# Optimization experiments

Hardware: AMD Instinct MI355X
Metric: run time of the kernel (lower is better)

## Reference

```python
import jax, jax.numpy as jnp
import numpy as np

N = 50000   # num_nodes
E = 800000  # num edges (COO)
T = 50      # timesteps
H = 64      # hidden_units


def setup_inputs() -> dict:
    key = jax.random.key(0)
    ks = jax.random.split(key, 16)
    s = 0.1  # weight init scale
    return {
        "features": jax.random.normal(ks[0], (1, T, N), jnp.float32),
        "index": jax.random.randint(ks[1], (E, 2), 0, N, jnp.int32),
        "value": jax.random.uniform(ks[2], (E,), jnp.float32),
        "W1_g": jax.random.normal(ks[3], (1 + H, 2 * H), jnp.float32) * s,
        "b1_g": jnp.ones((2 * H,), jnp.float32),
        "W1_c": jax.random.normal(ks[4], (1 + H, H), jnp.float32) * s,
        "b1_c": jnp.zeros((H,), jnp.float32),
        "W2b_g": jax.random.normal(ks[5], (H + 1, 2), jnp.float32) * s,
        "b2b_g": jnp.ones((2,), jnp.float32),
        "W2b_c": jax.random.normal(ks[6], (H + 1, 1), jnp.float32) * s,
        "b2b_c": jnp.zeros((1,), jnp.float32),
        "W2u_g": jax.random.normal(ks[7], (H + 1, 2), jnp.float32) * s,
        "b2u_g": jnp.ones((2,), jnp.float32),
        "W2u_c": jax.random.normal(ks[8], (H + 1, 1), jnp.float32) * s,
        "b2u_c": jnp.zeros((1,), jnp.float32),
    }


def _spmm(rows, cols, vals, X):
    # sparse COO adjacency (rows, cols, vals) @ dense X [N, d]
    return jax.ops.segment_sum(vals[:, None] * X[cols], rows, num_segments=N)


def _gru_layer(xs, rows, cols, vals, Wg, bg, Wc, bc, units):
    # xs: [T, N, d_in]; GCN-GRU cell scanned over time, batch=1
    h0 = jnp.zeros((N, units), xs.dtype)

    def step(h, x):
        def gconv(st, W, b):
            xc = jnp.concatenate([x, st], axis=-1)     # [N, d_in+units]
            return _spmm(rows, cols, vals, xc) @ W + b  # [N, out]

        ru = jax.nn.sigmoid(gconv(h, Wg, bg))
        r, u = jnp.split(ru, 2, axis=-1)
        c = jnp.tanh(gconv(r * h, Wc, bc))
        hn = u * h + (1.0 - u) * c
        return hn, hn

    _, hs = jax.lax.scan(step, h0, xs)
    return hs  # [T, N, units]


def reference(features, index, value, W1_g, b1_g, W1_c, b1_c,
              W2b_g, b2b_g, W2b_c, b2b_c, W2u_g, b2u_g, W2u_c, b2u_c):
    rows, cols = index[:, 0], index[:, 1]
    xs = features[0][..., None]  # [T, N, 1]
    # shared first layer (cell_1 is used by both multi-cell stacks)
    h1 = _gru_layer(xs, rows, cols, value, W1_g, b1_g, W1_c, b1_c, H)  # [T,N,H]
    out_b = _gru_layer(h1, rows, cols, value, W2b_g, b2b_g, W2b_c, b2b_c, 1)
    out_u = _gru_layer(h1, rows, cols, value, W2u_g, b2u_g, W2u_c, b2u_c, 1)
    # dynamic_rnn outputs: [batch=1, T, N]
    return out_b[..., 0][None], out_u[..., 0][None]
```

## Files before the change

### kernel.cpp

```cpp
#include <hip/hip_runtime.h>
#include <math.h>

#define NN 50000
#define EE 800000
#define TT 50

__device__ __forceinline__ float sigm(float x)   { return 1.f / (1.f + __expf(-x)); }
__device__ __forceinline__ float tanh_f(float x) { float e = __expf(2.f * x); return 1.f - 2.f / (e + 1.f); }


__global__ __launch_bounds__(256) void hist_kernel(const int* __restrict__ idx, int* __restrict__ cnt) {
    int e = blockIdx.x * blockDim.x + threadIdx.x;
    if (e < EE) atomicAdd(&cnt[idx[2 * e]], 1);
}

__global__ __launch_bounds__(1024) void scan_kernel(const int* __restrict__ cnt, int* __restrict__ rp) {
    __shared__ int part[1024];
    const int PER = (NN + 1023) / 1024;
    int t = threadIdx.x;
    int base = t * PER;
    int s = 0;
    for (int i = 0; i < PER; ++i) {
        int idx = base + i;
        if (idx < NN) s += cnt[idx];
    }
    part[t] = s;
    __syncthreads();
    int v = s;
    for (int off = 1; off < 1024; off <<= 1) {
        int add = (t >= off) ? part[t - off] : 0;
        __syncthreads();
        v += add;
        part[t] = v;
        __syncthreads();
    }
    int run = v - s;
    if (t == 0) rp[0] = 0;
    for (int i = 0; i < PER; ++i) {
        int idx = base + i;
        if (idx < NN) { run += cnt[idx]; rp[idx + 1] = run; }
    }
}

__global__ __launch_bounds__(256) void scatter_kernel(const int* __restrict__ idx, const float* __restrict__ val,
                                                      const int* __restrict__ rp, int* __restrict__ cnt,
                                                      int2* __restrict__ ev) {
    int e = blockIdx.x * blockDim.x + threadIdx.x;
    if (e >= EE) return;
    int r = idx[2 * e];
    int p = rp[r] + atomicAdd(&cnt[r], 1);
    ev[p] = make_int2(idx[2 * e + 1], __float_as_int(val[e]));
}


__global__ __launch_bounds__(256) void transpose_x(const float* __restrict__ F, float* __restrict__ xT) {
    __shared__ float tile[64][51];
    int n0 = blockIdx.x * 64;
    for (int i = threadIdx.x; i < TT * 64; i += 256) {
        int t = i >> 6, n = i & 63;
        if (n0 + n < NN) tile[n][t] = F[(size_t)t * NN + n0 + n];
    }
    __syncthreads();
    for (int i = threadIdx.x; i < 64 * 64; i += 256) {
        int n = i >> 6, t = i & 63;
        if (n0 + n < NN) xT[(size_t)(n0 + n) * 64 + t] = (t < TT) ? tile[n][t] : 0.f;
    }
}

__global__ __launch_bounds__(256) void spmm_sx(const int* __restrict__ rp, const int2* __restrict__ ev,
                                               const float* __restrict__ xT, float* __restrict__ SxAll) {
    int w = __builtin_amdgcn_readfirstlane((blockIdx.x * blockDim.x + threadIdx.x) >> 6);
    int lane = threadIdx.x & 63;
    if (w >= NN) return;
    int e0 = __builtin_amdgcn_readfirstlane(rp[w]);
    int e1 = __builtin_amdgcn_readfirstlane(rp[w + 1]);
    const float* xl = xT + lane;
    float a0 = 0.f, a1 = 0.f, a2 = 0.f, a3 = 0.f, a4 = 0.f, a5 = 0.f, a6 = 0.f, a7 = 0.f;
    int e = e0;
    for (; e + 8 <= e1; e += 8) {
        int2 q0 = ev[e + 0], q1 = ev[e + 1], q2 = ev[e + 2], q3 = ev[e + 3];
        int2 q4 = ev[e + 4], q5 = ev[e + 5], q6 = ev[e + 6], q7 = ev[e + 7];
        a0 = fmaf(__int_as_float(q0.y), xl[(size_t)q0.x * 64], a0);
        a1 = fmaf(__int_as_float(q1.y), xl[(size_t)q1.x * 64], a1);
        a2 = fmaf(__int_as_float(q2.y), xl[(size_t)q2.x * 64], a2);
        a3 = fmaf(__int_as_float(q3.y), xl[(size_t)q3.x * 64], a3);
        a4 = fmaf(__int_as_float(q4.y), xl[(size_t)q4.x * 64], a4);
        a5 = fmaf(__int_as_float(q5.y), xl[(size_t)q5.x * 64], a5);
        a6 = fmaf(__int_as_float(q6.y), xl[(size_t)q6.x * 64], a6);
        a7 = fmaf(__int_as_float(q7.y), xl[(size_t)q7.x * 64], a7);
    }
    for (; e < e1; ++e) {
        int2 q = ev[e];
        a0 = fmaf(__int_as_float(q.y), xl[(size_t)q.x * 64], a0);
    }
    float s = ((a0 + a1) + (a2 + a3)) + ((a4 + a5) + (a6 + a7));
    if (lane < TT) SxAll[(size_t)lane * NN + w] = s;
}


__global__ __launch_bounds__(256) void spmm64(const int* __restrict__ rp, const int2* __restrict__ ev,
                                              const float* __restrict__ Xin, float* __restrict__ Sout) {
    int w = __builtin_amdgcn_readfirstlane((blockIdx.x * blockDim.x + threadIdx.x) >> 6);
    int lane = threadIdx.x & 63;
    if (w >= NN) return;
    int e0 = __builtin_amdgcn_readfirstlane(rp[w]);
    int e1 = __builtin_amdgcn_readfirstlane(rp[w + 1]);
    const float* xl = Xin + lane;
    float a0 = 0.f, a1 = 0.f, a2 = 0.f, a3 = 0.f, a4 = 0.f, a5 = 0.f, a6 = 0.f, a7 = 0.f;
    int e = e0;
    for (; e + 8 <= e1; e += 8) {
        int2 q0 = ev[e + 0], q1 = ev[e + 1], q2 = ev[e + 2], q3 = ev[e + 3];
        int2 q4 = ev[e + 4], q5 = ev[e + 5], q6 = ev[e + 6], q7 = ev[e + 7];
        a0 = fmaf(__int_as_float(q0.y), xl[(size_t)q0.x * 64], a0);
        a1 = fmaf(__int_as_float(q1.y), xl[(size_t)q1.x * 64], a1);
        a2 = fmaf(__int_as_float(q2.y), xl[(size_t)q2.x * 64], a2);
        a3 = fmaf(__int_as_float(q3.y), xl[(size_t)q3.x * 64], a3);
        a4 = fmaf(__int_as_float(q4.y), xl[(size_t)q4.x * 64], a4);
        a5 = fmaf(__int_as_float(q5.y), xl[(size_t)q5.x * 64], a5);
        a6 = fmaf(__int_as_float(q6.y), xl[(size_t)q6.x * 64], a6);
        a7 = fmaf(__int_as_float(q7.y), xl[(size_t)q7.x * 64], a7);
    }
    for (; e < e1; ++e) {
        int2 q = ev[e];
        a0 = fmaf(__int_as_float(q.y), xl[(size_t)q.x * 64], a0);
    }
    Sout[(size_t)w * 64 + lane] = ((a0 + a1) + (a2 + a3)) + ((a4 + a5) + (a6 + a7));
}


__global__ __launch_bounds__(256) void cand_update(const float* __restrict__ S2, const float* __restrict__ Sx,
                                                   const float* __restrict__ Wc, const float* __restrict__ bc,
                                                   const float* __restrict__ u1, float* __restrict__ h1,
                                                   const float* __restrict__ Wbg, const float* __restrict__ Wbc,
                                                   const float* __restrict__ Wug, const float* __restrict__ Wuc,
                                                   float* __restrict__ z8) {
    int j = threadIdx.x & 63;
    int g = threadIdx.x >> 6;
    float w[65];
#pragma unroll
    for (int k = 0; k < 65; ++k) w[k] = Wc[k * 64 + j];
    float bj = bc[j];
    float wz0 = Wbg[j * 2], wz1 = Wbg[j * 2 + 1], wz2 = Wbc[j];
    float wz3 = Wug[j * 2], wz4 = Wug[j * 2 + 1], wz5 = Wuc[j];
    for (int n = blockIdx.x * 4 + g; n < NN; n += gridDim.x * 4) {
        float acc = fmaf(Sx[n], w[0], bj);
        const float4* s2 = (const float4*)(S2 + (size_t)n * 64);
#pragma unroll
        for (int q = 0; q < 16; ++q) {
            float4 sv = s2[q];
            acc = fmaf(sv.x, w[1 + 4 * q], acc);
            acc = fmaf(sv.y, w[2 + 4 * q], acc);
            acc = fmaf(sv.z, w[3 + 4 * q], acc);
            acc = fmaf(sv.w, w[4 + 4 * q], acc);
        }
        float c = tanh_f(acc);
        float u = u1[(size_t)n * 64 + j];
        float ho = h1[(size_t)n * 64 + j];
        float hn = fmaf(u, ho - c, c);
        h1[(size_t)n * 64 + j] = hn;
        float p0 = hn * wz0, p1 = hn * wz1, p2 = hn * wz2;
        float p3 = hn * wz3, p4 = hn * wz4, p5 = hn * wz5;
#pragma unroll
        for (int off = 1; off < 64; off <<= 1) {
            p0 += __shfl_xor(p0, off);
            p1 += __shfl_xor(p1, off);
            p2 += __shfl_xor(p2, off);
            p3 += __shfl_xor(p3, off);
            p4 += __shfl_xor(p4, off);
            p5 += __shfl_xor(p5, off);
        }
        if (j == 0) {
            z8[(size_t)n * 8 + 0] = p0; z8[(size_t)n * 8 + 1] = p1; z8[(size_t)n * 8 + 2] = p2;
            z8[(size_t)n * 8 + 3] = p3; z8[(size_t)n * 8 + 4] = p4; z8[(size_t)n * 8 + 5] = p5;
        }
    }
}


__global__ __launch_bounds__(256) void merged1(int GA,
        const int* __restrict__ rp, const int2* __restrict__ ev,
        const float* __restrict__ h1, float* __restrict__ Sh,
        const float* __restrict__ z8,
        const float* __restrict__ hb, const float* __restrict__ hu,
        const float* __restrict__ Wbg, const float* __restrict__ bbg,
        const float* __restrict__ Wug, const float* __restrict__ bug,
        float* __restrict__ z2, float* __restrict__ g2, float* __restrict__ S3c) {
    if ((int)blockIdx.x < GA) {
        int w = __builtin_amdgcn_readfirstlane(((int)blockIdx.x * 256 + (int)threadIdx.x) >> 6);
        int lane = threadIdx.x & 63;
        if (w >= NN) return;
        int e0 = __builtin_amdgcn_readfirstlane(rp[w]);
        int e1 = __builtin_amdgcn_readfirstlane(rp[w + 1]);
        const float* xl = h1 + lane;
        float a0 = 0.f, a1 = 0.f, a2 = 0.f, a3 = 0.f, a4 = 0.f, a5 = 0.f, a6 = 0.f, a7 = 0.f;
        int e = e0;
        for (; e + 8 <= e1; e += 8) {
            int2 q0 = ev[e + 0], q1 = ev[e + 1], q2 = ev[e + 2], q3 = ev[e + 3];
            int2 q4 = ev[e + 4], q5 = ev[e + 5], q6 = ev[e + 6], q7 = ev[e + 7];
            a0 = fmaf(__int_as_float(q0.y), xl[(size_t)q0.x * 64], a0);
            a1 = fmaf(__int_as_float(q1.y), xl[(size_t)q1.x * 64], a1);
            a2 = fmaf(__int_as_float(q2.y), xl[(size_t)q2.x * 64], a2);
            a3 = fmaf(__int_as_float(q3.y), xl[(size_t)q3.x * 64], a3);
            a4 = fmaf(__int_as_float(q4.y), xl[(size_t)q4.x * 64], a4);
            a5 = fmaf(__int_as_float(q5.y), xl[(size_t)q5.x * 64], a5);
            a6 = fmaf(__int_as_float(q6.y), xl[(size_t)q6.x * 64], a6);
            a7 = fmaf(__int_as_float(q7.y), xl[(size_t)q7.x * 64], a7);
        }
        for (; e < e1; ++e) {
            int2 q = ev[e];
            a0 = fmaf(__int_as_float(q.y), xl[(size_t)q.x * 64], a0);
        }
        Sh[(size_t)w * 64 + lane] = ((a0 + a1) + (a2 + a3)) + ((a4 + a5) + (a6 + a7));
    } else {
        int gid = ((int)blockIdx.x - GA) * 256 + threadIdx.x;
        int row = gid >> 3;
        int j = gid & 7;
        if (row >= NN) return;
        int e = rp[row], e1 = rp[row + 1];
        float a0 = 0.f, a1 = 0.f, a2 = 0.f, a3 = 0.f;
        for (; e + 3 < e1; e += 4) {
            int2 p0 = ev[e], p1 = ev[e + 1], p2 = ev[e + 2], p3 = ev[e + 3];
            a0 = fmaf(__int_as_float(p0.y), z8[(size_t)p0.x * 8 + j], a0);
            a1 = fmaf(__int_as_float(p1.y), z8[(size_t)p1.x * 8 + j], a1);
            a2 = fmaf(__int_as_float(p2.y), z8[(size_t)p2.x * 8 + j], a2);
            a3 = fmaf(__int_as_float(p3.y), z8[(size_t)p3.x * 8 + j], a3);
        }
        for (; e < e1; ++e) {
            int2 p = ev[e];
            a0 = fmaf(__int_as_float(p.y), z8[(size_t)p.x * 8 + j], a0);
        }
        float s = (a0 + a1) + (a2 + a3);
        if (j == 2) S3c[row * 2 + 0] = s;
        if (j == 5) S3c[row * 2 + 1] = s;
        int lane = threadIdx.x & 63;
        int base = lane & ~7;
        float s0 = __shfl(s, base + 0);
        float s1 = __shfl(s, base + 1);
        float s3 = __shfl(s, base + 3);
        float s4 = __shfl(s, base + 4);
        float s6 = __shfl(s, base + 6);
        float s7 = __shfl(s, base + 7);
        if (j == 0) {
            float rb = sigm(fmaf(s6, Wbg[128], s0) + bbg[0]);
            float ub = sigm(fmaf(s6, Wbg[129], s1) + bbg[1]);
            float ru = sigm(fmaf(s7, Wug[128], s3) + bug[0]);
            float uu = sigm(fmaf(s7, Wug[129], s4) + bug[1]);
            z2[row * 2 + 0] = rb * hb[row];
            z2[row * 2 + 1] = ru * hu[row];
            g2[row * 2 + 0] = ub;
            g2[row * 2 + 1] = uu;
        }
    }
}


#define G1_CHUNK 32
__global__ __launch_bounds__(128) void merged2(int GA,
        const float* __restrict__ Sh, const float* __restrict__ Sx,
        const float* __restrict__ Wg, const float* __restrict__ bg,
        const float* __restrict__ h1, float* __restrict__ rh, float* __restrict__ u1,
        const int* __restrict__ rp, const int2* __restrict__ ev,
        const float* __restrict__ z2, const float* __restrict__ S3c, const float* __restrict__ g2,
        const float* __restrict__ Wbc, const float* __restrict__ bbc,
        const float* __restrict__ Wuc, const float* __restrict__ buc,
        float* __restrict__ hb, float* __restrict__ hu,
        float* __restrict__ z8, float* __restrict__ out, int tPrev) {
    __shared__ float4 s4[G1_CHUNK][16];
    __shared__ float sxl[G1_CHUNK];
    if ((int)blockIdx.x < GA) {
        int j = threadIdx.x;
        float w0 = Wg[j];
        float wk[64];
#pragma unroll
        for (int k = 0; k < 64; ++k) wk[k] = Wg[(1 + k) * 128 + j];
        float bj = bg[j];
        int n0 = (int)blockIdx.x * G1_CHUNK;
        int nmax = min(G1_CHUNK, NN - n0);
        for (int idx = j; idx < G1_CHUNK * 16; idx += 128) {
            int n = idx >> 4, q = idx & 15;
            if (n < nmax) s4[n][q] = *(const float4*)(Sh + (size_t)(n0 + n) * 64 + q * 4);
        }
        if (j < G1_CHUNK && j < nmax) sxl[j] = Sx[n0 + j];
        __syncthreads();
        for (int n = 0; n < nmax; ++n) {
            float acc = fmaf(sxl[n], w0, bj);
#pragma unroll
            for (int q = 0; q < 16; ++q) {
                float4 sv = s4[n][q];
                acc = fmaf(sv.x, wk[4 * q + 0], acc);
                acc = fmaf(sv.y, wk[4 * q + 1], acc);
                acc = fmaf(sv.z, wk[4 * q + 2], acc);
                acc = fmaf(sv.w, wk[4 * q + 3], acc);
            }
            float g = sigm(acc);
            int node = n0 + n;
            if (j < 64) rh[(size_t)node * 64 + j] = g * h1[(size_t)node * 64 + j];
            else        u1[(size_t)node * 64 + (j - 64)] = g;
        }
    } else {
        int gid = ((int)blockIdx.x - GA) * 128 + threadIdx.x;
        int row = gid >> 1;
        int j = gid & 1;
        if (row >= NN) return;
        int e = rp[row], e1 = rp[row + 1];
        float a0 = 0.f, a1 = 0.f, a2 = 0.f, a3 = 0.f;
        for (; e + 3 < e1; e += 4) {
            int2 p0 = ev[e], p1 = ev[e + 1], p2 = ev[e + 2], p3 = ev[e + 3];
            a0 = fmaf(__int_as_float(p0.y), z2[(size_t)p0.x * 2 + j], a0);
            a1 = fmaf(__int_as_float(p1.y), z2[(size_t)p1.x * 2 + j], a1);
            a2 = fmaf(__int_as_float(p2.y), z2[(size_t)p2.x * 2 + j], a2);
            a3 = fmaf(__int_as_float(p3.y), z2[(size_t)p3.x * 2 + j], a3);
        }
        for (; e < e1; ++e) {
            int2 p = ev[e];
            a0 = fmaf(__int_as_float(p.y), z2[(size_t)p.x * 2 + j], a0);
        }
        float s = (a0 + a1) + (a2 + a3);
        int lane = threadIdx.x & 63;
        int base = lane & ~1;
        float sA = __shfl(s, base + 0);
        float sB = __shfl(s, base + 1);
        if (j == 0) {
            float cb = tanh_f(fmaf(sA, Wbc[64], S3c[row * 2 + 0]) + bbc[0]);
            float cu = tanh_f(fmaf(sB, Wuc[64], S3c[row * 2 + 1]) + buc[0]);
            float ub = g2[row * 2 + 0], uu = g2[row * 2 + 1];
            float hbn = fmaf(ub, hb[row] - cb, cb);
            float hun = fmaf(uu, hu[row] - cu, cu);
            hb[row] = hbn; hu[row] = hun;
            z8[(size_t)row * 8 + 6] = hbn;
            z8[(size_t)row * 8 + 7] = hun;
            out[(size_t)tPrev * NN + row] = hbn;
            out[(size_t)(TT + tPrev) * NN + row] = hun;
        }
    }
}


extern "C" void kernel_launch(void* const* d_in, const int* in_sizes, int n_in,
                              void* d_out, int out_size, void* d_ws, size_t ws_size,
                              hipStream_t stream) {
    const float* features = (const float*)d_in[0];
    const int*   index    = (const int*)d_in[1];
    const float* value    = (const float*)d_in[2];
    const float* W1g  = (const float*)d_in[3];
    const float* b1g  = (const float*)d_in[4];
    const float* W1c  = (const float*)d_in[5];
    const float* b1c  = (const float*)d_in[6];
    const float* W2bg = (const float*)d_in[7];
    const float* b2bg = (const float*)d_in[8];
    const float* W2bc = (const float*)d_in[9];
    const float* b2bc = (const float*)d_in[10];
    const float* W2ug = (const float*)d_in[11];
    const float* b2ug = (const float*)d_in[12];
    const float* W2uc = (const float*)d_in[13];
    const float* b2uc = (const float*)d_in[14];
    float* out = (float*)d_out;

    char* ws = (char*)d_ws;
    size_t o = 0;
    auto alloc = [&](size_t bytes) { size_t cur = o; o += (bytes + 255) & ~(size_t)255; return cur; };
    size_t o_h1  = alloc((size_t)NN * 64 * 4);
    size_t o_hb  = alloc((size_t)NN * 4);
    size_t o_hu  = alloc((size_t)NN * 4);
    size_t o_z8  = alloc((size_t)NN * 8 * 4);
    size_t zeroEnd = o;
    size_t o_rp  = alloc((size_t)(NN + 1) * 4);
    size_t o_cnt = alloc((size_t)NN * 4);
    size_t o_ev  = alloc((size_t)EE * 8);
    size_t o_Sh  = alloc((size_t)NN * 64 * 4);
    size_t o_SxA = alloc((size_t)TT * NN * 4);
    size_t o_rh  = alloc((size_t)NN * 64 * 4);
    size_t o_u1  = alloc((size_t)NN * 64 * 4);
    size_t o_S2  = alloc((size_t)NN * 64 * 4);
    size_t o_S3c = alloc((size_t)NN * 2 * 4);
    size_t o_z2  = alloc((size_t)NN * 2 * 4);
    size_t o_g2  = alloc((size_t)NN * 2 * 4);
    (void)ws_size; (void)in_sizes; (void)n_in; (void)out_size;

    float* h1  = (float*)(ws + o_h1);
    float* hb  = (float*)(ws + o_hb);
    float* hu  = (float*)(ws + o_hu);
    float* z8  = (float*)(ws + o_z8);
    int*   rp  = (int*)(ws + o_rp);
    int*   cnt = (int*)(ws + o_cnt);
    int2*  ev  = (int2*)(ws + o_ev);
    float* Sh  = (float*)(ws + o_Sh);
    float* SxA = (float*)(ws + o_SxA);
    float* rh  = (float*)(ws + o_rh);
    float* u1  = (float*)(ws + o_u1);
    float* S2  = (float*)(ws + o_S2);
    float* S3c = (float*)(ws + o_S3c);
    float* z2  = (float*)(ws + o_z2);
    float* g2  = (float*)(ws + o_g2);
    float* xT  = S2;

    (void)hipMemsetAsync(ws + o_cnt, 0, (size_t)NN * 4, stream);
    hist_kernel<<<(EE + 255) / 256, 256, 0, stream>>>(index, cnt);
    scan_kernel<<<1, 1024, 0, stream>>>(cnt, rp);
    (void)hipMemsetAsync(ws + o_cnt, 0, (size_t)NN * 4, stream);
    scatter_kernel<<<(EE + 255) / 256, 256, 0, stream>>>(index, value, rp, cnt, ev);

    (void)hipMemsetAsync(ws + o_h1, 0, zeroEnd - o_h1, stream);
    (void)hipMemsetAsync(ws + o_Sh, 0, (size_t)NN * 64 * 4, stream);

    transpose_x<<<(NN + 63) / 64, 256, 0, stream>>>(features, xT);
    spmm_sx<<<(NN + 3) / 4, 256, 0, stream>>>(rp, ev, xT, SxA);

    const int GA1 = (NN + 3) / 4;
    const int GB1 = (NN * 8 + 255) / 256;
    const int GA2 = (NN + G1_CHUNK - 1) / G1_CHUNK;
    const int GB2 = (NN * 2 + 127) / 128;

    for (int t = 0; t < TT; ++t) {
        const float* Sxt = SxA + (size_t)t * NN;
        int g2grid = (t > 0) ? (GA2 + GB2) : GA2;
        merged2<<<g2grid, 128, 0, stream>>>(GA2, Sh, Sxt, W1g, b1g, h1, rh, u1,
                                            rp, ev, z2, S3c, g2, W2bc, b2bc, W2uc, b2uc,
                                            hb, hu, z8, out, t - 1);
        spmm64<<<(NN + 3) / 4, 256, 0, stream>>>(rp, ev, rh, S2);
        cand_update<<<1024, 256, 0, stream>>>(S2, Sxt, W1c, b1c, u1, h1, W2bg, W2bc, W2ug, W2uc, z8);
        int gA = (t < TT - 1) ? GA1 : 0;
        merged1<<<gA + GB1, 256, 0, stream>>>(gA, rp, ev, h1, Sh,
                                              z8, hb, hu, W2bg, b2bg, W2ug, b2ug, z2, g2, S3c);
    }
    merged2<<<GB2, 128, 0, stream>>>(0, Sh, SxA, W1g, b1g, h1, rh, u1,
                                     rp, ev, z2, S3c, g2, W2bc, b2bc, W2uc, b2uc,
                                     hb, hu, z8, out, TT - 1);
}
```

Baseline: 7.534 ms.

## Fuse candidate SpMM with GRU update and pad CSR rows to multiples of eight

Each CSR row is padded to a multiple of 8 entries. The padding slots are zero-filled, so they read column 0 with weight 0. This lets every SpMM drop its scalar tail loop. The separate spmm64 and cand_update kernels are merged into one spmm_cand kernel: each wave computes its row's aggregated r*h in LDS and immediately applies the candidate weights, which are also held in LDS. That removes the S2 buffer round trip and one launch per timestep. The single-block prefix scan is also replaced with a three-kernel block scan, at the cost of roughly a fifth more gather traffic from the padding entries.

```diff
diff --git a/kernel.cpp b/kernel.cpp
--- a/kernel.cpp
+++ b/kernel.cpp
@@ -4,6 +4,8 @@
 #define NN 50000
 #define EE 800000
 #define TT 50
+#define EVCAP 1150016
+#define SB 196
 
 __device__ __forceinline__ float sigm(float x)   { return 1.f / (1.f + __expf(-x)); }
 __device__ __forceinline__ float tanh_f(float x) { float e = __expf(2.f * x); return 1.f - 2.f / (e + 1.f); }
@@ -14,32 +16,46 @@
     if (e < EE) atomicAdd(&cnt[idx[2 * e]], 1);
 }
 
-__global__ __launch_bounds__(1024) void scan_kernel(const int* __restrict__ cnt, int* __restrict__ rp) {
-    __shared__ int part[1024];
-    const int PER = (NN + 1023) / 1024;
+__global__ __launch_bounds__(256) void scan1(const int* __restrict__ cnt, int* __restrict__ rp,
+                                             int* __restrict__ bsum) {
+    __shared__ int s[256];
     int t = threadIdx.x;
-    int base = t * PER;
-    int s = 0;
-    for (int i = 0; i < PER; ++i) {
-        int idx = base + i;
-        if (idx < NN) s += cnt[idx];
-    }
-    part[t] = s;
+    int g = blockIdx.x * 256 + t;
+    int v = (g < NN) ? ((cnt[g] + 7) & ~7) : 0;
+    s[t] = v;
     __syncthreads();
-    int v = s;
-    for (int off = 1; off < 1024; off <<= 1) {
-        int add = (t >= off) ? part[t - off] : 0;
+    for (int off = 1; off < 256; off <<= 1) {
+        int add = (t >= off) ? s[t - off] : 0;
         __syncthreads();
         v += add;
-        part[t] = v;
+        s[t] = v;
         __syncthreads();
     }
-    int run = v - s;
-    if (t == 0) rp[0] = 0;
-    for (int i = 0; i < PER; ++i) {
-        int idx = base + i;
-        if (idx < NN) { run += cnt[idx]; rp[idx + 1] = run; }
-    }
+    if (g < NN) rp[g + 1] = v;
+    if (t == 255) bsum[blockIdx.x] = v;
+}
+
+__global__ __launch_bounds__(256) void scan2(int* __restrict__ bsum) {
+    __shared__ int s[256];
+    int t = threadIdx.x;
+    int v = (t < SB) ? bsum[t] : 0;
+    s[t] = v;
+    __syncthreads();
+    for (int off = 1; off < 256; off <<= 1) {
+        int add = (t >= off) ? s[t - off] : 0;
+        __syncthreads();
+        v += add;
+        s[t] = v;
+        __syncthreads();
+    }
+    if (t < SB) bsum[t] = v;
+}
+
+__global__ __launch_bounds__(256) void scan3(int* __restrict__ rp, const int* __restrict__ bsum) {
+    int g = blockIdx.x * 256 + threadIdx.x;
+    int off = (blockIdx.x > 0) ? bsum[blockIdx.x - 1] : 0;
+    if (g < NN) rp[g + 1] += off;
+    if (g == 0) rp[0] = 0;
 }
 
 __global__ __launch_bounds__(256) void scatter_kernel(const int* __restrict__ idx, const float* __restrict__ val,
@@ -72,12 +88,11 @@
     int w = __builtin_amdgcn_readfirstlane((blockIdx.x * blockDim.x + threadIdx.x) >> 6);
     int lane = threadIdx.x & 63;
     if (w >= NN) return;
-    int e0 = __builtin_amdgcn_readfirstlane(rp[w]);
+    int e  = __builtin_amdgcn_readfirstlane(rp[w]);
     int e1 = __builtin_amdgcn_readfirstlane(rp[w + 1]);
     const float* xl = xT + lane;
     float a0 = 0.f, a1 = 0.f, a2 = 0.f, a3 = 0.f, a4 = 0.f, a5 = 0.f, a6 = 0.f, a7 = 0.f;
-    int e = e0;
-    for (; e + 8 <= e1; e += 8) {
+    for (; e < e1; e += 8) {
         int2 q0 = ev[e + 0], q1 = ev[e + 1], q2 = ev[e + 2], q3 = ev[e + 3];
         int2 q4 = ev[e + 4], q5 = ev[e + 5], q6 = ev[e + 6], q7 = ev[e + 7];
         a0 = fmaf(__int_as_float(q0.y), xl[(size_t)q0.x * 64], a0);
@@ -89,75 +104,60 @@
         a6 = fmaf(__int_as_float(q6.y), xl[(size_t)q6.x * 64], a6);
         a7 = fmaf(__int_as_float(q7.y), xl[(size_t)q7.x * 64], a7);
     }
-    for (; e < e1; ++e) {
-        int2 q = ev[e];
-        a0 = fmaf(__int_as_float(q.y), xl[(size_t)q.x * 64], a0);
-    }
     float s = ((a0 + a1) + (a2 + a3)) + ((a4 + a5) + (a6 + a7));
     if (lane < TT) SxAll[(size_t)lane * NN + w] = s;
 }
 
 
-__global__ __launch_bounds__(256) void spmm64(const int* __restrict__ rp, const int2* __restrict__ ev,
-                                              const float* __restrict__ Xin, float* __restrict__ Sout) {
-    int w = __builtin_amdgcn_readfirstlane((blockIdx.x * blockDim.x + threadIdx.x) >> 6);
-    int lane = threadIdx.x & 63;
-    if (w >= NN) return;
-    int e0 = __builtin_amdgcn_readfirstlane(rp[w]);
-    int e1 = __builtin_amdgcn_readfirstlane(rp[w + 1]);
-    const float* xl = Xin + lane;
-    float a0 = 0.f, a1 = 0.f, a2 = 0.f, a3 = 0.f, a4 = 0.f, a5 = 0.f, a6 = 0.f, a7 = 0.f;
-    int e = e0;
-    for (; e + 8 <= e1; e += 8) {
-        int2 q0 = ev[e + 0], q1 = ev[e + 1], q2 = ev[e + 2], q3 = ev[e + 3];
-        int2 q4 = ev[e + 4], q5 = ev[e + 5], q6 = ev[e + 6], q7 = ev[e + 7];
-        a0 = fmaf(__int_as_float(q0.y), xl[(size_t)q0.x * 64], a0);
-        a1 = fmaf(__int_as_float(q1.y), xl[(size_t)q1.x * 64], a1);
-        a2 = fmaf(__int_as_float(q2.y), xl[(size_t)q2.x * 64], a2);
-        a3 = fmaf(__int_as_float(q3.y), xl[(size_t)q3.x * 64], a3);
-        a4 = fmaf(__int_as_float(q4.y), xl[(size_t)q4.x * 64], a4);
-        a5 = fmaf(__int_as_float(q5.y), xl[(size_t)q5.x * 64], a5);
-        a6 = fmaf(__int_as_float(q6.y), xl[(size_t)q6.x * 64], a6);
-        a7 = fmaf(__int_as_float(q7.y), xl[(size_t)q7.x * 64], a7);
-    }
-    for (; e < e1; ++e) {
-        int2 q = ev[e];
-        a0 = fmaf(__int_as_float(q.y), xl[(size_t)q.x * 64], a0);
-    }
-    Sout[(size_t)w * 64 + lane] = ((a0 + a1) + (a2 + a3)) + ((a4 + a5) + (a6 + a7));
-}
-
-
-__global__ __launch_bounds__(256) void cand_update(const float* __restrict__ S2, const float* __restrict__ Sx,
-                                                   const float* __restrict__ Wc, const float* __restrict__ bc,
-                                                   const float* __restrict__ u1, float* __restrict__ h1,
-                                                   const float* __restrict__ Wbg, const float* __restrict__ Wbc,
-                                                   const float* __restrict__ Wug, const float* __restrict__ Wuc,
-                                                   float* __restrict__ z8) {
-    int j = threadIdx.x & 63;
-    int g = threadIdx.x >> 6;
-    float w[65];
-#pragma unroll
-    for (int k = 0; k < 65; ++k) w[k] = Wc[k * 64 + j];
+__global__ __launch_bounds__(256) void spmm_cand(const int* __restrict__ rp, const int2* __restrict__ ev,
+        const float* __restrict__ rh, const float* __restrict__ Sx,
+        const float* __restrict__ Wc, const float* __restrict__ bc,
+        const float* __restrict__ u1, float* __restrict__ h1,
+        const float* __restrict__ Wbg, const float* __restrict__ Wbc,
+        const float* __restrict__ Wug, const float* __restrict__ Wuc,
+        float* __restrict__ z8) {
+    __shared__ float ldsW[65 * 64];
+    __shared__ float ldsS[4][64];
+    int t = threadIdx.x;
+    for (int i = t; i < 65 * 16; i += 256)
+        ((float4*)ldsW)[i] = ((const float4*)Wc)[i];
+    __syncthreads();
+    int lane = t & 63;
+    int wv = t >> 6;
+    int j = lane;
     float bj = bc[j];
     float wz0 = Wbg[j * 2], wz1 = Wbg[j * 2 + 1], wz2 = Wbc[j];
     float wz3 = Wug[j * 2], wz4 = Wug[j * 2 + 1], wz5 = Wuc[j];
-    for (int n = blockIdx.x * 4 + g; n < NN; n += gridDim.x * 4) {
-        float acc = fmaf(Sx[n], w[0], bj);
-        const float4* s2 = (const float4*)(S2 + (size_t)n * 64);
-#pragma unroll
-        for (int q = 0; q < 16; ++q) {
-            float4 sv = s2[q];
-            acc = fmaf(sv.x, w[1 + 4 * q], acc);
-            acc = fmaf(sv.y, w[2 + 4 * q], acc);
-            acc = fmaf(sv.z, w[3 + 4 * q], acc);
-            acc = fmaf(sv.w, w[4 + 4 * q], acc);
-        }
+    int wstride = gridDim.x * 4;
+    for (int wi = blockIdx.x * 4 + wv; wi < NN; wi += wstride) {
+        int w = __builtin_amdgcn_readfirstlane(wi);
+        int e  = __builtin_amdgcn_readfirstlane(rp[w]);
+        int e1 = __builtin_amdgcn_readfirstlane(rp[w + 1]);
+        const float* xl = rh + lane;
+        float a0 = 0.f, a1 = 0.f, a2 = 0.f, a3 = 0.f, a4 = 0.f, a5 = 0.f, a6 = 0.f, a7 = 0.f;
+        for (; e < e1; e += 8) {
+            int2 q0 = ev[e + 0], q1 = ev[e + 1], q2 = ev[e + 2], q3 = ev[e + 3];
+            int2 q4 = ev[e + 4], q5 = ev[e + 5], q6 = ev[e + 6], q7 = ev[e + 7];
+            a0 = fmaf(__int_as_float(q0.y), xl[(size_t)q0.x * 64], a0);
+            a1 = fmaf(__int_as_float(q1.y), xl[(size_t)q1.x * 64], a1);
+            a2 = fmaf(__int_as_float(q2.y), xl[(size_t)q2.x * 64], a2);
+            a3 = fmaf(__int_as_float(q3.y), xl[(size_t)q3.x * 64], a3);
+            a4 = fmaf(__int_as_float(q4.y), xl[(size_t)q4.x * 64], a4);
+            a5 = fmaf(__int_as_float(q5.y), xl[(size_t)q5.x * 64], a5);
+            a6 = fmaf(__int_as_float(q6.y), xl[(size_t)q6.x * 64], a6);
+            a7 = fmaf(__int_as_float(q7.y), xl[(size_t)q7.x * 64], a7);
+        }
+        float s2 = ((a0 + a1) + (a2 + a3)) + ((a4 + a5) + (a6 + a7));
+        ldsS[wv][lane] = s2;
+        float acc = fmaf(Sx[w], ldsW[j], bj);
+#pragma unroll 8
+        for (int k = 0; k < 64; ++k)
+            acc = fmaf(ldsS[wv][k], ldsW[(k + 1) * 64 + j], acc);
         float c = tanh_f(acc);
-        float u = u1[(size_t)n * 64 + j];
-        float ho = h1[(size_t)n * 64 + j];
+        float u  = u1[(size_t)w * 64 + j];
+        float ho = h1[(size_t)w * 64 + j];
         float hn = fmaf(u, ho - c, c);
-        h1[(size_t)n * 64 + j] = hn;
+        h1[(size_t)w * 64 + j] = hn;
         float p0 = hn * wz0, p1 = hn * wz1, p2 = hn * wz2;
         float p3 = hn * wz3, p4 = hn * wz4, p5 = hn * wz5;
 #pragma unroll
@@ -170,8 +170,8 @@
             p5 += __shfl_xor(p5, off);
         }
         if (j == 0) {
-            z8[(size_t)n * 8 + 0] = p0; z8[(size_t)n * 8 + 1] = p1; z8[(size_t)n * 8 + 2] = p2;
-            z8[(size_t)n * 8 + 3] = p3; z8[(size_t)n * 8 + 4] = p4; z8[(size_t)n * 8 + 5] = p5;
+            z8[(size_t)w * 8 + 0] = p0; z8[(size_t)w * 8 + 1] = p1; z8[(size_t)w * 8 + 2] = p2;
+            z8[(size_t)w * 8 + 3] = p3; z8[(size_t)w * 8 + 4] = p4; z8[(size_t)w * 8 + 5] = p5;
         }
     }
 }
@@ -189,12 +189,11 @@
         int w = __builtin_amdgcn_readfirstlane(((int)blockIdx.x * 256 + (int)threadIdx.x) >> 6);
         int lane = threadIdx.x & 63;
         if (w >= NN) return;
-        int e0 = __builtin_amdgcn_readfirstlane(rp[w]);
+        int e  = __builtin_amdgcn_readfirstlane(rp[w]);
         int e1 = __builtin_amdgcn_readfirstlane(rp[w + 1]);
         const float* xl = h1 + lane;
         float a0 = 0.f, a1 = 0.f, a2 = 0.f, a3 = 0.f, a4 = 0.f, a5 = 0.f, a6 = 0.f, a7 = 0.f;
-        int e = e0;
-        for (; e + 8 <= e1; e += 8) {
+        for (; e < e1; e += 8) {
             int2 q0 = ev[e + 0], q1 = ev[e + 1], q2 = ev[e + 2], q3 = ev[e + 3];
             int2 q4 = ev[e + 4], q5 = ev[e + 5], q6 = ev[e + 6], q7 = ev[e + 7];
             a0 = fmaf(__int_as_float(q0.y), xl[(size_t)q0.x * 64], a0);
@@ -205,10 +204,6 @@
             a5 = fmaf(__int_as_float(q5.y), xl[(size_t)q5.x * 64], a5);
             a6 = fmaf(__int_as_float(q6.y), xl[(size_t)q6.x * 64], a6);
             a7 = fmaf(__int_as_float(q7.y), xl[(size_t)q7.x * 64], a7);
-        }
-        for (; e < e1; ++e) {
-            int2 q = ev[e];
-            a0 = fmaf(__int_as_float(q.y), xl[(size_t)q.x * 64], a0);
         }
         Sh[(size_t)w * 64 + lane] = ((a0 + a1) + (a2 + a3)) + ((a4 + a5) + (a6 + a7));
     } else {
@@ -366,12 +361,12 @@
     size_t zeroEnd = o;
     size_t o_rp  = alloc((size_t)(NN + 1) * 4);
     size_t o_cnt = alloc((size_t)NN * 4);
-    size_t o_ev  = alloc((size_t)EE * 8);
+    size_t o_bs  = alloc((size_t)256 * 4);
+    size_t o_ev  = alloc((size_t)EVCAP * 8);
     size_t o_Sh  = alloc((size_t)NN * 64 * 4);
     size_t o_SxA = alloc((size_t)TT * NN * 4);
     size_t o_rh  = alloc((size_t)NN * 64 * 4);
     size_t o_u1  = alloc((size_t)NN * 64 * 4);
-    size_t o_S2  = alloc((size_t)NN * 64 * 4);
     size_t o_S3c = alloc((size_t)NN * 2 * 4);
     size_t o_z2  = alloc((size_t)NN * 2 * 4);
     size_t o_g2  = alloc((size_t)NN * 2 * 4);
@@ -383,21 +378,24 @@
     float* z8  = (float*)(ws + o_z8);
     int*   rp  = (int*)(ws + o_rp);
     int*   cnt = (int*)(ws + o_cnt);
+    int*   bsum = (int*)(ws + o_bs);
     int2*  ev  = (int2*)(ws + o_ev);
     float* Sh  = (float*)(ws + o_Sh);
     float* SxA = (float*)(ws + o_SxA);
     float* rh  = (float*)(ws + o_rh);
     float* u1  = (float*)(ws + o_u1);
-    float* S2  = (float*)(ws + o_S2);
     float* S3c = (float*)(ws + o_S3c);
     float* z2  = (float*)(ws + o_z2);
     float* g2  = (float*)(ws + o_g2);
-    float* xT  = S2;
+    float* xT  = rh;
 
     (void)hipMemsetAsync(ws + o_cnt, 0, (size_t)NN * 4, stream);
     hist_kernel<<<(EE + 255) / 256, 256, 0, stream>>>(index, cnt);
-    scan_kernel<<<1, 1024, 0, stream>>>(cnt, rp);
+    scan1<<<SB, 256, 0, stream>>>(cnt, rp, bsum);
+    scan2<<<1, 256, 0, stream>>>(bsum);
+    scan3<<<SB, 256, 0, stream>>>(rp, bsum);
     (void)hipMemsetAsync(ws + o_cnt, 0, (size_t)NN * 4, stream);
+    (void)hipMemsetAsync(ws + o_ev, 0, (size_t)EVCAP * 8, stream);
     scatter_kernel<<<(EE + 255) / 256, 256, 0, stream>>>(index, value, rp, cnt, ev);
 
     (void)hipMemsetAsync(ws + o_h1, 0, zeroEnd - o_h1, stream);
@@ -417,8 +415,8 @@
         merged2<<<g2grid, 128, 0, stream>>>(GA2, Sh, Sxt, W1g, b1g, h1, rh, u1,
                                             rp, ev, z2, S3c, g2, W2bc, b2bc, W2uc, b2uc,
                                             hb, hu, z8, out, t - 1);
-        spmm64<<<(NN + 3) / 4, 256, 0, stream>>>(rp, ev, rh, S2);
-        cand_update<<<1024, 256, 0, stream>>>(S2, Sxt, W1c, b1c, u1, h1, W2bg, W2bc, W2ug, W2uc, z8);
+        spmm_cand<<<2048, 256, 0, stream>>>(rp, ev, rh, Sxt, W1c, b1c, u1, h1,
+                                            W2bg, W2bc, W2ug, W2uc, z8);
         int gA = (t < TT - 1) ? GA1 : 0;
         merged1<<<gA + GB1, 256, 0, stream>>>(gA, rp, ev, h1, Sh,
                                               z8, hb, hu, W2bg, b2bg, W2ug, b2ug, z2, g2, S3c);
```

Result: faster. 6.255 ms (-17.0%).
